# Performance work log

Measured on AMD Instinct MI355X. Metric: run time of the kernel, lower is better.

Reference implementation:

```python
import jax, jax.numpy as jnp
import numpy as np

M_SIZE = 128          # local window half-size
SCALING = 1.0 / np.sqrt(64.0)


def _window_allowed(seq_len, m):
    """Boolean [L, L] mask; True where attention is allowed.

    Matches torch window_mask: window width = 2m+1; rows near the edges are
    clamped so every row sees exactly `2m+1` columns.
    """
    size = 2 * m + 1
    if seq_len <= size:
        return jnp.ones((seq_len, seq_len), dtype=bool)
    rows = jnp.arange(seq_len)[:, None]            # [L,1]
    cols = jnp.arange(seq_len)[None, :]            # [1,L]
    start = jnp.clip(rows - m, 0, seq_len - size)  # [L,1]
    return (cols >= start) & (cols < start + size)


def setup_inputs() -> dict:
    key = jax.random.key(0)
    kq, kk, kv = jax.random.split(key, 3)
    B, L, D = 8, 4096, 64
    q = jax.random.normal(kq, (B, L, D), dtype=jnp.float32)
    k = jax.random.normal(kk, (B, L, D), dtype=jnp.float32)
    v = jax.random.normal(kv, (B, L, D), dtype=jnp.float32)
    return {"q": q, "k": k, "v": v}


def reference(q, k, v):
    # scores: [B, Lq, Lk]
    scores = jnp.einsum("bqd,bkd->bqk", q, k) * SCALING
    allowed = _window_allowed(q.shape[1], M_SIZE)          # [L, L]
    scores = jnp.where(allowed[None, :, :], scores, -jnp.inf)
    attention = jax.nn.softmax(scores, axis=2)
    out = jnp.einsum("bqk,bkv->bqv", attention, v)
    return (out, attention)
```

## Files before the change

kernel.cpp:

```cpp
#include <hip/hip_runtime.h>
#include <math.h>

#define L_SEQ 4096
#define D_HEAD 64
#define M_WIN 128
#define WIN 257
#define QB 8
#define W 264
#define WF4 66
#define ATTS 272
#define SCALE 0.125f

#define RL(v, i) __uint_as_float(__builtin_amdgcn_readlane(__float_as_uint(v), (i)))

static __device__ __forceinline__ unsigned bfr(float x) {
    unsigned u = __float_as_uint(x);
    return (u + 0x7fffu + ((u >> 16) & 1u)) >> 16;
}
static __device__ __forceinline__ unsigned bfpack(float lo, float hi) {
    return bfr(lo) | (bfr(hi) << 16);
}

__global__ __launch_bounds__(256, 3) void win_attn_kernel(
    const float* __restrict__ Q, const float* __restrict__ K,
    const float* __restrict__ V, float* __restrict__ OutO,
    float* __restrict__ OutA)
{
    extern __shared__ float smem[];
    uint4* k_su = (uint4*)smem;
    float* att  = smem + 2112 * 4;

    const int t  = threadIdx.x;
    const int w  = t >> 6;
    const int ln = t & 63;

    const int bid = blockIdx.x;
    const int b   = bid >> 9;
    const int q0  = (bid & 511) * QB;

    int s0 = q0 - M_WIN;
    if (s0 < 0) s0 = 0;
    if (s0 > L_SEQ - WIN) s0 = L_SEQ - WIN;
    const int wcount = (L_SEQ - s0 < W) ? (L_SEQ - s0) : W;

    {
        const float4* Kg = (const float4*)(K + ((size_t)(b * L_SEQ + s0)) * D_HEAD);
        #pragma unroll 3
        for (int idx = t; idx < 264 * 8; idx += 256) {
            int row = idx >> 3, c8 = idx & 7;
            int gr  = (row < wcount) ? row : wcount - 1;
            float4 a  = Kg[(size_t)gr * 16 + c8 * 2];
            float4 bb = Kg[(size_t)gr * 16 + c8 * 2 + 1];
            uint4 d;
            d.x = bfpack(a.x, a.y);   d.y = bfpack(a.z, a.w);
            d.z = bfpack(bb.x, bb.y); d.w = bfpack(bb.z, bb.w);
            k_su[row * 8 + (c8 ^ (row & 7))] = d;
        }
    }
    const int r0g = q0 + 2 * w;
    const float qv0 = Q[((size_t)(b * L_SEQ) + r0g)     * D_HEAD + ln];
    const float qv1 = Q[((size_t)(b * L_SEQ) + r0g + 1) * D_HEAD + ln];
    if (ln < 16) {
        int r = 2 * w + (ln >> 3);
        att[r * ATTS + 264 + (ln & 7)] = 0.f;
    }
    __syncthreads();

    float p0[5], p1[5];
    {
        const uint4* kp[5];
        int msk[5];
        #pragma unroll
        for (int cg = 0; cg < 5; ++cg) {
            int colr = cg * 64 + ln;
            int col  = (colr < W) ? colr : W - 1;
            kp[cg]  = k_su + (size_t)col * 8;
            msk[cg] = col & 7;
            p0[cg] = 0.f; p1[cg] = 0.f;
        }
        #pragma unroll
        for (int c8 = 0; c8 < 8; ++c8) {
            float a0 = RL(qv0, 8*c8+0), a1 = RL(qv0, 8*c8+1),
                  a2 = RL(qv0, 8*c8+2), a3 = RL(qv0, 8*c8+3),
                  a4 = RL(qv0, 8*c8+4), a5 = RL(qv0, 8*c8+5),
                  a6 = RL(qv0, 8*c8+6), a7 = RL(qv0, 8*c8+7);
            float b0 = RL(qv1, 8*c8+0), b1 = RL(qv1, 8*c8+1),
                  b2 = RL(qv1, 8*c8+2), b3 = RL(qv1, 8*c8+3),
                  b4 = RL(qv1, 8*c8+4), b5 = RL(qv1, 8*c8+5),
                  b6 = RL(qv1, 8*c8+6), b7 = RL(qv1, 8*c8+7);
            #pragma unroll
            for (int cg = 0; cg < 5; ++cg) {
                uint4 kk = kp[cg][c8 ^ msk[cg]];
                float e0 = __uint_as_float(kk.x << 16);
                float e1 = __uint_as_float(kk.x & 0xffff0000u);
                float e2 = __uint_as_float(kk.y << 16);
                float e3 = __uint_as_float(kk.y & 0xffff0000u);
                float e4 = __uint_as_float(kk.z << 16);
                float e5 = __uint_as_float(kk.z & 0xffff0000u);
                float e6 = __uint_as_float(kk.w << 16);
                float e7 = __uint_as_float(kk.w & 0xffff0000u);
                p0[cg] += a0*e0 + a1*e1 + a2*e2 + a3*e3
                        + a4*e4 + a5*e5 + a6*e6 + a7*e7;
                p1[cg] += b0*e0 + b1*e1 + b2*e2 + b3*e3
                        + b4*e4 + b5*e5 + b6*e6 + b7*e7;
            }
        }
        #pragma unroll
        for (int cg = 0; cg < 5; ++cg) { p0[cg] *= SCALE; p1[cg] *= SCALE; }
    }

    {
        int st0 = r0g - M_WIN;
        if (st0 < 0) st0 = 0;
        if (st0 > L_SEQ - WIN) st0 = L_SEQ - WIN;
        const int lo0 = st0 - s0;
        int st1 = r0g + 1 - M_WIN;
        if (st1 < 0) st1 = 0;
        if (st1 > L_SEQ - WIN) st1 = L_SEQ - WIN;
        const int lo1 = st1 - s0;

        float m0 = -1e30f, m1 = -1e30f;
        #pragma unroll
        for (int cg = 0; cg < 5; ++cg) {
            int colr = cg * 64 + ln;
            bool in0 = (colr >= lo0) && (colr < lo0 + WIN);
            bool in1 = (colr >= lo1) && (colr < lo1 + WIN);
            p0[cg] = in0 ? p0[cg] : -1e30f;
            p1[cg] = in1 ? p1[cg] : -1e30f;
            m0 = fmaxf(m0, p0[cg]);
            m1 = fmaxf(m1, p1[cg]);
        }
        #pragma unroll
        for (int off = 32; off >= 1; off >>= 1) {
            m0 = fmaxf(m0, __shfl_xor(m0, off));
            m1 = fmaxf(m1, __shfl_xor(m1, off));
        }
        float sum0 = 0.f, sum1 = 0.f;
        #pragma unroll
        for (int cg = 0; cg < 5; ++cg) {
            float e0 = (p0[cg] <= -1e29f) ? 0.f : __expf(p0[cg] - m0);
            float e1 = (p1[cg] <= -1e29f) ? 0.f : __expf(p1[cg] - m1);
            p0[cg] = e0; p1[cg] = e1;
            sum0 += e0; sum1 += e1;
        }
        #pragma unroll
        for (int off = 32; off >= 1; off >>= 1) {
            sum0 += __shfl_xor(sum0, off);
            sum1 += __shfl_xor(sum1, off);
        }
        const float inv0 = 1.f / sum0, inv1 = 1.f / sum1;
        #pragma unroll
        for (int cg = 0; cg < 5; ++cg) {
            int colr = cg * 64 + ln;
            if (colr < W) {
                att[(2 * w)     * ATTS + colr] = p0[cg] * inv0;
                att[(2 * w + 1) * ATTS + colr] = p1[cg] * inv1;
            }
        }
    }

    {
        const int cq = ln >> 4;
        const int dg = ln & 15;
        const float4* Vg4 = (const float4*)(V + ((size_t)(b * L_SEQ + s0)) * D_HEAD);
        const float4* a4r0 = (const float4*)(att + (2 * w) * ATTS);
        const float4* a4r1 = (const float4*)(att + (2 * w + 1) * ATTS);
        float4 acc0 = {0.f,0.f,0.f,0.f}, acc1 = {0.f,0.f,0.f,0.f};
        #pragma unroll 2
        for (int G = 0; G < 17; ++G) {
            float4 pa = a4r0[4 * G + cq];
            float4 pb = a4r1[4 * G + cq];
            #pragma unroll
            for (int e = 0; e < 4; ++e) {
                int col  = 16 * G + 4 * cq + e;
                int colc = (col < wcount) ? col : wcount - 1;
                float4 vv = Vg4[(size_t)colc * 16 + dg];
                float fa = (e == 0) ? pa.x : (e == 1) ? pa.y : (e == 2) ? pa.z : pa.w;
                float fb = (e == 0) ? pb.x : (e == 1) ? pb.y : (e == 2) ? pb.z : pb.w;
                acc0.x += fa * vv.x; acc0.y += fa * vv.y;
                acc0.z += fa * vv.z; acc0.w += fa * vv.w;
                acc1.x += fb * vv.x; acc1.y += fb * vv.y;
                acc1.z += fb * vv.z; acc1.w += fb * vv.w;
            }
        }
        #pragma unroll
        for (int off = 16; off <= 32; off <<= 1) {
            acc0.x += __shfl_xor(acc0.x, off); acc0.y += __shfl_xor(acc0.y, off);
            acc0.z += __shfl_xor(acc0.z, off); acc0.w += __shfl_xor(acc0.w, off);
            acc1.x += __shfl_xor(acc1.x, off); acc1.y += __shfl_xor(acc1.y, off);
            acc1.z += __shfl_xor(acc1.z, off); acc1.w += __shfl_xor(acc1.w, off);
        }
        if (ln < 16) {
            float4* o4 = (float4*)(OutO + ((size_t)(b * L_SEQ + r0g)) * D_HEAD);
            o4[dg]      = acc0;
            o4[16 + dg] = acc1;
        }
    }

    if ((s0 & 3) == 0) {
        const int zlo = s0 >> 2;
        #pragma unroll
        for (int r = 0; r < 2; ++r) {
            float4* rowp = (float4*)(OutA + ((size_t)(b * L_SEQ + r0g + r)) * L_SEQ);
            const float4* arow = (const float4*)(att + (2 * w + r) * ATTS);
            #pragma unroll 4
            for (int j = 0; j < 16; ++j) {
                int f4i = j * 64 + ln;
                int u4  = f4i - zlo;
                float4 wv = {0.f,0.f,0.f,0.f};
                if (u4 >= 0 && u4 < WF4) wv = arow[u4];
                rowp[f4i] = wv;
            }
        }
    } else {
        #pragma unroll
        for (int r = 0; r < 2; ++r) {
            float4* rowp = (float4*)(OutA + ((size_t)(b * L_SEQ + r0g + r)) * L_SEQ);
            const float* arow = att + (2 * w + r) * ATTS;
            #pragma unroll 2
            for (int j = 0; j < 16; ++j) {
                int f4i = j * 64 + ln;
                int u   = 4 * f4i - s0;
                float4 wv;
                wv.x = (u     >= 0 && u     < W) ? arow[u]     : 0.f;
                wv.y = (u + 1 >= 0 && u + 1 < W) ? arow[u + 1] : 0.f;
                wv.z = (u + 2 >= 0 && u + 2 < W) ? arow[u + 2] : 0.f;
                wv.w = (u + 3 >= 0 && u + 3 < W) ? arow[u + 3] : 0.f;
                rowp[f4i] = wv;
            }
        }
    }
}

extern "C" void kernel_launch(void* const* d_in, const int* in_sizes, int n_in,
                              void* d_out, int out_size, void* d_ws, size_t ws_size,
                              hipStream_t stream) {
    const float* Q = (const float*)d_in[0];
    const float* K = (const float*)d_in[1];
    const float* V = (const float*)d_in[2];
    float* OutO = (float*)d_out;
    float* OutA = OutO + (size_t)8 * L_SEQ * D_HEAD;

    const int smem_bytes = 2112 * 16 + QB * ATTS * 4;
    hipFuncSetAttribute((const void*)win_attn_kernel,
                        hipFuncAttributeMaxDynamicSharedMemorySize, smem_bytes);

    dim3 grid(8 * (L_SEQ / QB));
    dim3 block(256);
    win_attn_kernel<<<grid, block, smem_bytes, stream>>>(Q, K, V, OutO, OutA);
}
```

Baseline: 168.3 us.

## Process four query sub-tiles per block to reuse staged K window

Each block now handles 32 queries in four sequential sub-tiles, loading a 288-row bf16 K window into shared memory once and indexing into it per sub-tile. This amortizes the K global load and bf16 conversion across more queries. It reduces the grid from 4096 to 1024 blocks, lowering available parallelism and serializing the attention-row writes per block.

```diff
diff --git a/kernel.cpp b/kernel.cpp
--- a/kernel.cpp
+++ b/kernel.cpp
@@ -6,6 +6,9 @@
 #define M_WIN 128
 #define WIN 257
 #define QB 8
+#define NT 4
+#define QBLK 32
+#define KROWS 288
 #define W 264
 #define WF4 66
 #define ATTS 272
@@ -28,205 +31,214 @@
 {
     extern __shared__ float smem[];
     uint4* k_su = (uint4*)smem;
-    float* att  = smem + 2112 * 4;
+    float* att  = smem + 2304 * 4;
 
     const int t  = threadIdx.x;
     const int w  = t >> 6;
     const int ln = t & 63;
-
     const int bid = blockIdx.x;
-    const int b   = bid >> 9;
-    const int q0  = (bid & 511) * QB;
-
-    int s0 = q0 - M_WIN;
-    if (s0 < 0) s0 = 0;
-    if (s0 > L_SEQ - WIN) s0 = L_SEQ - WIN;
-    const int wcount = (L_SEQ - s0 < W) ? (L_SEQ - s0) : W;
+    const int b      = bid >> 7;
+    const int q0_blk = (bid & 127) * QBLK;
+
+    int s0_blk = q0_blk - M_WIN;
+    if (s0_blk < 0) s0_blk = 0;
+    if (s0_blk > L_SEQ - KROWS) s0_blk = L_SEQ - KROWS;
 
     {
-        const float4* Kg = (const float4*)(K + ((size_t)(b * L_SEQ + s0)) * D_HEAD);
+        const float4* Kg = (const float4*)(K + ((size_t)(b * L_SEQ + s0_blk)) * D_HEAD);
         #pragma unroll 3
-        for (int idx = t; idx < 264 * 8; idx += 256) {
+        for (int idx = t; idx < KROWS * 8; idx += 256) {
             int row = idx >> 3, c8 = idx & 7;
-            int gr  = (row < wcount) ? row : wcount - 1;
-            float4 a  = Kg[(size_t)gr * 16 + c8 * 2];
-            float4 bb = Kg[(size_t)gr * 16 + c8 * 2 + 1];
+            float4 a  = Kg[(size_t)row * 16 + c8 * 2];
+            float4 bb = Kg[(size_t)row * 16 + c8 * 2 + 1];
             uint4 d;
             d.x = bfpack(a.x, a.y);   d.y = bfpack(a.z, a.w);
             d.z = bfpack(bb.x, bb.y); d.w = bfpack(bb.z, bb.w);
             k_su[row * 8 + (c8 ^ (row & 7))] = d;
         }
     }
-    const int r0g = q0 + 2 * w;
-    const float qv0 = Q[((size_t)(b * L_SEQ) + r0g)     * D_HEAD + ln];
-    const float qv1 = Q[((size_t)(b * L_SEQ) + r0g + 1) * D_HEAD + ln];
     if (ln < 16) {
         int r = 2 * w + (ln >> 3);
         att[r * ATTS + 264 + (ln & 7)] = 0.f;
     }
     __syncthreads();
 
-    float p0[5], p1[5];
-    {
-        const uint4* kp[5];
-        int msk[5];
-        #pragma unroll
-        for (int cg = 0; cg < 5; ++cg) {
-            int colr = cg * 64 + ln;
-            int col  = (colr < W) ? colr : W - 1;
-            kp[cg]  = k_su + (size_t)col * 8;
-            msk[cg] = col & 7;
-            p0[cg] = 0.f; p1[cg] = 0.f;
-        }
-        #pragma unroll
-        for (int c8 = 0; c8 < 8; ++c8) {
-            float a0 = RL(qv0, 8*c8+0), a1 = RL(qv0, 8*c8+1),
-                  a2 = RL(qv0, 8*c8+2), a3 = RL(qv0, 8*c8+3),
-                  a4 = RL(qv0, 8*c8+4), a5 = RL(qv0, 8*c8+5),
-                  a6 = RL(qv0, 8*c8+6), a7 = RL(qv0, 8*c8+7);
-            float b0 = RL(qv1, 8*c8+0), b1 = RL(qv1, 8*c8+1),
-                  b2 = RL(qv1, 8*c8+2), b3 = RL(qv1, 8*c8+3),
-                  b4 = RL(qv1, 8*c8+4), b5 = RL(qv1, 8*c8+5),
-                  b6 = RL(qv1, 8*c8+6), b7 = RL(qv1, 8*c8+7);
-            #pragma unroll
-            for (int cg = 0; cg < 5; ++cg) {
-                uint4 kk = kp[cg][c8 ^ msk[cg]];
-                float e0 = __uint_as_float(kk.x << 16);
-                float e1 = __uint_as_float(kk.x & 0xffff0000u);
-                float e2 = __uint_as_float(kk.y << 16);
-                float e3 = __uint_as_float(kk.y & 0xffff0000u);
-                float e4 = __uint_as_float(kk.z << 16);
-                float e5 = __uint_as_float(kk.z & 0xffff0000u);
-                float e6 = __uint_as_float(kk.w << 16);
-                float e7 = __uint_as_float(kk.w & 0xffff0000u);
-                p0[cg] += a0*e0 + a1*e1 + a2*e2 + a3*e3
-                        + a4*e4 + a5*e5 + a6*e6 + a7*e7;
-                p1[cg] += b0*e0 + b1*e1 + b2*e2 + b3*e3
-                        + b4*e4 + b5*e5 + b6*e6 + b7*e7;
-            }
-        }
-        #pragma unroll
-        for (int cg = 0; cg < 5; ++cg) { p0[cg] *= SCALE; p1[cg] *= SCALE; }
-    }
-
-    {
-        int st0 = r0g - M_WIN;
-        if (st0 < 0) st0 = 0;
-        if (st0 > L_SEQ - WIN) st0 = L_SEQ - WIN;
-        const int lo0 = st0 - s0;
-        int st1 = r0g + 1 - M_WIN;
-        if (st1 < 0) st1 = 0;
-        if (st1 > L_SEQ - WIN) st1 = L_SEQ - WIN;
-        const int lo1 = st1 - s0;
-
-        float m0 = -1e30f, m1 = -1e30f;
-        #pragma unroll
-        for (int cg = 0; cg < 5; ++cg) {
-            int colr = cg * 64 + ln;
-            bool in0 = (colr >= lo0) && (colr < lo0 + WIN);
-            bool in1 = (colr >= lo1) && (colr < lo1 + WIN);
-            p0[cg] = in0 ? p0[cg] : -1e30f;
-            p1[cg] = in1 ? p1[cg] : -1e30f;
-            m0 = fmaxf(m0, p0[cg]);
-            m1 = fmaxf(m1, p1[cg]);
-        }
-        #pragma unroll
-        for (int off = 32; off >= 1; off >>= 1) {
-            m0 = fmaxf(m0, __shfl_xor(m0, off));
-            m1 = fmaxf(m1, __shfl_xor(m1, off));
-        }
-        float sum0 = 0.f, sum1 = 0.f;
-        #pragma unroll
-        for (int cg = 0; cg < 5; ++cg) {
-            float e0 = (p0[cg] <= -1e29f) ? 0.f : __expf(p0[cg] - m0);
-            float e1 = (p1[cg] <= -1e29f) ? 0.f : __expf(p1[cg] - m1);
-            p0[cg] = e0; p1[cg] = e1;
-            sum0 += e0; sum1 += e1;
-        }
-        #pragma unroll
-        for (int off = 32; off >= 1; off >>= 1) {
-            sum0 += __shfl_xor(sum0, off);
-            sum1 += __shfl_xor(sum1, off);
-        }
-        const float inv0 = 1.f / sum0, inv1 = 1.f / sum1;
-        #pragma unroll
-        for (int cg = 0; cg < 5; ++cg) {
-            int colr = cg * 64 + ln;
-            if (colr < W) {
-                att[(2 * w)     * ATTS + colr] = p0[cg] * inv0;
-                att[(2 * w + 1) * ATTS + colr] = p1[cg] * inv1;
-            }
-        }
-    }
-
-    {
-        const int cq = ln >> 4;
-        const int dg = ln & 15;
-        const float4* Vg4 = (const float4*)(V + ((size_t)(b * L_SEQ + s0)) * D_HEAD);
-        const float4* a4r0 = (const float4*)(att + (2 * w) * ATTS);
-        const float4* a4r1 = (const float4*)(att + (2 * w + 1) * ATTS);
-        float4 acc0 = {0.f,0.f,0.f,0.f}, acc1 = {0.f,0.f,0.f,0.f};
-        #pragma unroll 2
-        for (int G = 0; G < 17; ++G) {
-            float4 pa = a4r0[4 * G + cq];
-            float4 pb = a4r1[4 * G + cq];
-            #pragma unroll
-            for (int e = 0; e < 4; ++e) {
-                int col  = 16 * G + 4 * cq + e;
-                int colc = (col < wcount) ? col : wcount - 1;
-                float4 vv = Vg4[(size_t)colc * 16 + dg];
-                float fa = (e == 0) ? pa.x : (e == 1) ? pa.y : (e == 2) ? pa.z : pa.w;
-                float fb = (e == 0) ? pb.x : (e == 1) ? pb.y : (e == 2) ? pb.z : pb.w;
-                acc0.x += fa * vv.x; acc0.y += fa * vv.y;
-                acc0.z += fa * vv.z; acc0.w += fa * vv.w;
-                acc1.x += fb * vv.x; acc1.y += fb * vv.y;
-                acc1.z += fb * vv.z; acc1.w += fb * vv.w;
-            }
-        }
-        #pragma unroll
-        for (int off = 16; off <= 32; off <<= 1) {
-            acc0.x += __shfl_xor(acc0.x, off); acc0.y += __shfl_xor(acc0.y, off);
-            acc0.z += __shfl_xor(acc0.z, off); acc0.w += __shfl_xor(acc0.w, off);
-            acc1.x += __shfl_xor(acc1.x, off); acc1.y += __shfl_xor(acc1.y, off);
-            acc1.z += __shfl_xor(acc1.z, off); acc1.w += __shfl_xor(acc1.w, off);
-        }
-        if (ln < 16) {
-            float4* o4 = (float4*)(OutO + ((size_t)(b * L_SEQ + r0g)) * D_HEAD);
-            o4[dg]      = acc0;
-            o4[16 + dg] = acc1;
-        }
-    }
-
-    if ((s0 & 3) == 0) {
-        const int zlo = s0 >> 2;
-        #pragma unroll
-        for (int r = 0; r < 2; ++r) {
-            float4* rowp = (float4*)(OutA + ((size_t)(b * L_SEQ + r0g + r)) * L_SEQ);
-            const float4* arow = (const float4*)(att + (2 * w + r) * ATTS);
-            #pragma unroll 4
-            for (int j = 0; j < 16; ++j) {
-                int f4i = j * 64 + ln;
-                int u4  = f4i - zlo;
-                float4 wv = {0.f,0.f,0.f,0.f};
-                if (u4 >= 0 && u4 < WF4) wv = arow[u4];
-                rowp[f4i] = wv;
-            }
-        }
-    } else {
-        #pragma unroll
-        for (int r = 0; r < 2; ++r) {
-            float4* rowp = (float4*)(OutA + ((size_t)(b * L_SEQ + r0g + r)) * L_SEQ);
-            const float* arow = att + (2 * w + r) * ATTS;
+    #pragma unroll 1
+    for (int ti = 0; ti < NT; ++ti) {
+        const int q0  = q0_blk + ti * QB;
+        const int r0g = q0 + 2 * w;
+        int s0 = q0 - M_WIN;
+        if (s0 < 0) s0 = 0;
+        if (s0 > L_SEQ - WIN) s0 = L_SEQ - WIN;
+        const int off    = s0 - s0_blk;
+        const int wcount = (L_SEQ - s0 < W) ? (L_SEQ - s0) : W;
+
+        const float qv0 = Q[((size_t)(b * L_SEQ) + r0g)     * D_HEAD + ln];
+        const float qv1 = Q[((size_t)(b * L_SEQ) + r0g + 1) * D_HEAD + ln];
+
+        float p0[5], p1[5];
+        {
+            const uint4* kp[5];
+            int msk[5];
+            #pragma unroll
+            for (int cg = 0; cg < 5; ++cg) {
+                int colr = cg * 64 + ln;
+                int col  = (colr < wcount) ? colr : wcount - 1;
+                int row  = off + col;
+                kp[cg]  = k_su + (size_t)row * 8;
+                msk[cg] = row & 7;
+                p0[cg] = 0.f; p1[cg] = 0.f;
+            }
+            #pragma unroll
+            for (int c8 = 0; c8 < 8; ++c8) {
+                float a0 = RL(qv0, 8*c8+0), a1 = RL(qv0, 8*c8+1),
+                      a2 = RL(qv0, 8*c8+2), a3 = RL(qv0, 8*c8+3),
+                      a4 = RL(qv0, 8*c8+4), a5 = RL(qv0, 8*c8+5),
+                      a6 = RL(qv0, 8*c8+6), a7 = RL(qv0, 8*c8+7);
+                float b0 = RL(qv1, 8*c8+0), b1 = RL(qv1, 8*c8+1),
+                      b2 = RL(qv1, 8*c8+2), b3 = RL(qv1, 8*c8+3),
+                      b4 = RL(qv1, 8*c8+4), b5 = RL(qv1, 8*c8+5),
+                      b6 = RL(qv1, 8*c8+6), b7 = RL(qv1, 8*c8+7);
+                #pragma unroll
+                for (int cg = 0; cg < 5; ++cg) {
+                    uint4 kk = kp[cg][c8 ^ msk[cg]];
+                    float e0 = __uint_as_float(kk.x << 16);
+                    float e1 = __uint_as_float(kk.x & 0xffff0000u);
+                    float e2 = __uint_as_float(kk.y << 16);
+                    float e3 = __uint_as_float(kk.y & 0xffff0000u);
+                    float e4 = __uint_as_float(kk.z << 16);
+                    float e5 = __uint_as_float(kk.z & 0xffff0000u);
+                    float e6 = __uint_as_float(kk.w << 16);
+                    float e7 = __uint_as_float(kk.w & 0xffff0000u);
+                    p0[cg] += a0*e0 + a1*e1 + a2*e2 + a3*e3
+                            + a4*e4 + a5*e5 + a6*e6 + a7*e7;
+                    p1[cg] += b0*e0 + b1*e1 + b2*e2 + b3*e3
+                            + b4*e4 + b5*e5 + b6*e6 + b7*e7;
+                }
+            }
+            #pragma unroll
+            for (int cg = 0; cg < 5; ++cg) { p0[cg] *= SCALE; p1[cg] *= SCALE; }
+        }
+
+        {
+            int st0 = r0g - M_WIN;
+            if (st0 < 0) st0 = 0;
+            if (st0 > L_SEQ - WIN) st0 = L_SEQ - WIN;
+            const int lo0 = st0 - s0;
+            int st1 = r0g + 1 - M_WIN;
+            if (st1 < 0) st1 = 0;
+            if (st1 > L_SEQ - WIN) st1 = L_SEQ - WIN;
+            const int lo1 = st1 - s0;
+
+            float m0 = -1e30f, m1 = -1e30f;
+            #pragma unroll
+            for (int cg = 0; cg < 5; ++cg) {
+                int colr = cg * 64 + ln;
+                bool in0 = (colr >= lo0) && (colr < lo0 + WIN) && (colr < wcount);
+                bool in1 = (colr >= lo1) && (colr < lo1 + WIN) && (colr < wcount);
+                p0[cg] = in0 ? p0[cg] : -1e30f;
+                p1[cg] = in1 ? p1[cg] : -1e30f;
+                m0 = fmaxf(m0, p0[cg]);
+                m1 = fmaxf(m1, p1[cg]);
+            }
+            #pragma unroll
+            for (int off2 = 32; off2 >= 1; off2 >>= 1) {
+                m0 = fmaxf(m0, __shfl_xor(m0, off2));
+                m1 = fmaxf(m1, __shfl_xor(m1, off2));
+            }
+            float sum0 = 0.f, sum1 = 0.f;
+            #pragma unroll
+            for (int cg = 0; cg < 5; ++cg) {
+                float e0 = (p0[cg] <= -1e29f) ? 0.f : __expf(p0[cg] - m0);
+                float e1 = (p1[cg] <= -1e29f) ? 0.f : __expf(p1[cg] - m1);
+                p0[cg] = e0; p1[cg] = e1;
+                sum0 += e0; sum1 += e1;
+            }
+            #pragma unroll
+            for (int off2 = 32; off2 >= 1; off2 >>= 1) {
+                sum0 += __shfl_xor(sum0, off2);
+                sum1 += __shfl_xor(sum1, off2);
+            }
+            const float inv0 = 1.f / sum0, inv1 = 1.f / sum1;
+            #pragma unroll
+            for (int cg = 0; cg < 5; ++cg) {
+                int colr = cg * 64 + ln;
+                if (colr < W) {
+                    att[(2 * w)     * ATTS + colr] = p0[cg] * inv0;
+                    att[(2 * w + 1) * ATTS + colr] = p1[cg] * inv1;
+                }
+            }
+        }
+
+        {
+            const int cq = ln >> 4;
+            const int dg = ln & 15;
+            const float4* Vg4 = (const float4*)(V + ((size_t)(b * L_SEQ + s0)) * D_HEAD);
+            const float4* a4r0 = (const float4*)(att + (2 * w) * ATTS);
+            const float4* a4r1 = (const float4*)(att + (2 * w + 1) * ATTS);
+            float4 acc0 = {0.f,0.f,0.f,0.f}, acc1 = {0.f,0.f,0.f,0.f};
             #pragma unroll 2
-            for (int j = 0; j < 16; ++j) {
-                int f4i = j * 64 + ln;
-                int u   = 4 * f4i - s0;
-                float4 wv;
-                wv.x = (u     >= 0 && u     < W) ? arow[u]     : 0.f;
-                wv.y = (u + 1 >= 0 && u + 1 < W) ? arow[u + 1] : 0.f;
-                wv.z = (u + 2 >= 0 && u + 2 < W) ? arow[u + 2] : 0.f;
-                wv.w = (u + 3 >= 0 && u + 3 < W) ? arow[u + 3] : 0.f;
-                rowp[f4i] = wv;
+            for (int G = 0; G < 17; ++G) {
+                float4 pa = a4r0[4 * G + cq];
+                float4 pb = a4r1[4 * G + cq];
+                #pragma unroll
+                for (int e = 0; e < 4; ++e) {
+                    int col  = 16 * G + 4 * cq + e;
+                    int colc = (col < wcount) ? col : wcount - 1;
+                    float4 vv = Vg4[(size_t)colc * 16 + dg];
+                    float fa = (e == 0) ? pa.x : (e == 1) ? pa.y : (e == 2) ? pa.z : pa.w;
+                    float fb = (e == 0) ? pb.x : (e == 1) ? pb.y : (e == 2) ? pb.z : pb.w;
+                    acc0.x += fa * vv.x; acc0.y += fa * vv.y;
+                    acc0.z += fa * vv.z; acc0.w += fa * vv.w;
+                    acc1.x += fb * vv.x; acc1.y += fb * vv.y;
+                    acc1.z += fb * vv.z; acc1.w += fb * vv.w;
+                }
+            }
+            #pragma unroll
+            for (int off2 = 16; off2 <= 32; off2 <<= 1) {
+                acc0.x += __shfl_xor(acc0.x, off2); acc0.y += __shfl_xor(acc0.y, off2);
+                acc0.z += __shfl_xor(acc0.z, off2); acc0.w += __shfl_xor(acc0.w, off2);
+                acc1.x += __shfl_xor(acc1.x, off2); acc1.y += __shfl_xor(acc1.y, off2);
+                acc1.z += __shfl_xor(acc1.z, off2); acc1.w += __shfl_xor(acc1.w, off2);
+            }
+            if (ln < 16) {
+                float4* o4 = (float4*)(OutO + ((size_t)(b * L_SEQ + r0g)) * D_HEAD);
+                o4[dg]      = acc0;
+                o4[16 + dg] = acc1;
+            }
+        }
+
+        if ((s0 & 3) == 0) {
+            const int zlo = s0 >> 2;
+            #pragma unroll
+            for (int r = 0; r < 2; ++r) {
+                float4* rowp = (float4*)(OutA + ((size_t)(b * L_SEQ + r0g + r)) * L_SEQ);
+                const float4* arow = (const float4*)(att + (2 * w + r) * ATTS);
+                #pragma unroll 4
+                for (int j = 0; j < 16; ++j) {
+                    int f4i = j * 64 + ln;
+                    int u4  = f4i - zlo;
+                    float4 wv = {0.f,0.f,0.f,0.f};
+                    if (u4 >= 0 && u4 < WF4) wv = arow[u4];
+                    rowp[f4i] = wv;
+                }
+            }
+        } else {
+            #pragma unroll
+            for (int r = 0; r < 2; ++r) {
+                float4* rowp = (float4*)(OutA + ((size_t)(b * L_SEQ + r0g + r)) * L_SEQ);
+                const float* arow = att + (2 * w + r) * ATTS;
+                #pragma unroll 2
+                for (int j = 0; j < 16; ++j) {
+                    int f4i = j * 64 + ln;
+                    int u   = 4 * f4i - s0;
+                    float4 wv;
+                    wv.x = (u     >= 0 && u     < W) ? arow[u]     : 0.f;
+                    wv.y = (u + 1 >= 0 && u + 1 < W) ? arow[u + 1] : 0.f;
+                    wv.z = (u + 2 >= 0 && u + 2 < W) ? arow[u + 2] : 0.f;
+                    wv.w = (u + 3 >= 0 && u + 3 < W) ? arow[u + 3] : 0.f;
+                    rowp[f4i] = wv;
+                }
             }
         }
     }
@@ -241,11 +253,11 @@
     float* OutO = (float*)d_out;
     float* OutA = OutO + (size_t)8 * L_SEQ * D_HEAD;
 
-    const int smem_bytes = 2112 * 16 + QB * ATTS * 4;
+    const int smem_bytes = KROWS * 128 + QB * ATTS * 4;
     hipFuncSetAttribute((const void*)win_attn_kernel,
                         hipFuncAttributeMaxDynamicSharedMemorySize, smem_bytes);
 
-    dim3 grid(8 * (L_SEQ / QB));
+    dim3 grid(8 * (L_SEQ / QBLK));
     dim3 block(256);
     win_attn_kernel<<<grid, block, smem_bytes, stream>>>(Q, K, V, OutO, OutA);
 }
```

After: 172.7 us. +2.6%, slower.

## Add a fifth wavefront dedicated to zero-filling attention rows outside the window

Applied to the files above, without the earlier changes.

Grows the block from four to five wavefronts. The extra wavefront writes only the zero regions of the attention output rows and then exits, while the compute wavefronts store only the in-window band. This moves the bulk of the zero-store traffic off the critical compute warps so it overlaps with the QK/softmax/PV work. The unaligned-s0 branch hardcodes its band start at float4 index 959, which only holds for the clamped last window. The larger block may also change occupancy.

```diff
diff --git a/kernel.cpp b/kernel.cpp
--- a/kernel.cpp
+++ b/kernel.cpp
@@ -21,7 +21,7 @@
     return bfr(lo) | (bfr(hi) << 16);
 }
 
-__global__ __launch_bounds__(256, 3) void win_attn_kernel(
+__global__ __launch_bounds__(320, 3) void win_attn_kernel(
     const float* __restrict__ Q, const float* __restrict__ K,
     const float* __restrict__ V, float* __restrict__ OutO,
     float* __restrict__ OutA)
@@ -33,7 +33,6 @@
     const int t  = threadIdx.x;
     const int w  = t >> 6;
     const int ln = t & 63;
-
     const int bid = blockIdx.x;
     const int b   = bid >> 9;
     const int q0  = (bid & 511) * QB;
@@ -42,11 +41,13 @@
     if (s0 < 0) s0 = 0;
     if (s0 > L_SEQ - WIN) s0 = L_SEQ - WIN;
     const int wcount = (L_SEQ - s0 < W) ? (L_SEQ - s0) : W;
+    const int zlo = s0 >> 2;
+    const int zhi = (s0 & 3) ? 1024 : (zlo + WF4);
 
     {
         const float4* Kg = (const float4*)(K + ((size_t)(b * L_SEQ + s0)) * D_HEAD);
-        #pragma unroll 3
-        for (int idx = t; idx < 264 * 8; idx += 256) {
+        #pragma unroll 2
+        for (int idx = t; idx < 264 * 8; idx += 320) {
             int row = idx >> 3, c8 = idx & 7;
             int gr  = (row < wcount) ? row : wcount - 1;
             float4 a  = Kg[(size_t)gr * 16 + c8 * 2];
@@ -58,13 +59,30 @@
         }
     }
     const int r0g = q0 + 2 * w;
-    const float qv0 = Q[((size_t)(b * L_SEQ) + r0g)     * D_HEAD + ln];
-    const float qv1 = Q[((size_t)(b * L_SEQ) + r0g + 1) * D_HEAD + ln];
-    if (ln < 16) {
-        int r = 2 * w + (ln >> 3);
-        att[r * ATTS + 264 + (ln & 7)] = 0.f;
+    float qv0 = 0.f, qv1 = 0.f;
+    if (w < 4) {
+        qv0 = Q[((size_t)(b * L_SEQ) + r0g)     * D_HEAD + ln];
+        qv1 = Q[((size_t)(b * L_SEQ) + r0g + 1) * D_HEAD + ln];
+        if (ln < 16) {
+            int r = 2 * w + (ln >> 3);
+            att[r * ATTS + 264 + (ln & 7)] = 0.f;
+        }
     }
     __syncthreads();
+
+    if (w == 4) {
+        const float4 z = {0.f, 0.f, 0.f, 0.f};
+        #pragma unroll 4
+        for (int idx = ln; idx < QB * 1024; idx += 64) {
+            int ql  = idx >> 10;
+            int f4i = idx & 1023;
+            if (f4i < zlo || f4i >= zhi) {
+                float4* rowp = (float4*)(OutA + ((size_t)(b * L_SEQ + q0 + ql)) * L_SEQ);
+                rowp[f4i] = z;
+            }
+        }
+        return;
+    }
 
     float p0[5], p1[5];
     {
@@ -198,28 +216,20 @@
     }
 
     if ((s0 & 3) == 0) {
-        const int zlo = s0 >> 2;
         #pragma unroll
         for (int r = 0; r < 2; ++r) {
             float4* rowp = (float4*)(OutA + ((size_t)(b * L_SEQ + r0g + r)) * L_SEQ);
             const float4* arow = (const float4*)(att + (2 * w + r) * ATTS);
-            #pragma unroll 4
-            for (int j = 0; j < 16; ++j) {
-                int f4i = j * 64 + ln;
-                int u4  = f4i - zlo;
-                float4 wv = {0.f,0.f,0.f,0.f};
-                if (u4 >= 0 && u4 < WF4) wv = arow[u4];
-                rowp[f4i] = wv;
-            }
+            for (int i = ln; i < WF4; i += 64)
+                rowp[zlo + i] = arow[i];
         }
     } else {
         #pragma unroll
         for (int r = 0; r < 2; ++r) {
             float4* rowp = (float4*)(OutA + ((size_t)(b * L_SEQ + r0g + r)) * L_SEQ);
             const float* arow = att + (2 * w + r) * ATTS;
-            #pragma unroll 2
-            for (int j = 0; j < 16; ++j) {
-                int f4i = j * 64 + ln;
+            for (int i = ln; i < 65; i += 64) {
+                int f4i = 959 + i;
                 int u   = 4 * f4i - s0;
                 float4 wv;
                 wv.x = (u     >= 0 && u     < W) ? arow[u]     : 0.f;
@@ -246,6 +256,6 @@
                         hipFuncAttributeMaxDynamicSharedMemorySize, smem_bytes);
 
     dim3 grid(8 * (L_SEQ / QB));
-    dim3 block(256);
+    dim3 block(320);
     win_attn_kernel<<<grid, block, smem_bytes, stream>>>(Q, K, V, OutO, OutA);
 }
```

New measurement: 194.8 us. 1.16x slower.
